# Performance work log

Hardware: AMD Instinct MI355X
Metric: run time of the kernel (lower is better)

Reference implementation:

```python
import jax, jax.numpy as jnp
import numpy as np

N_NODES = 50000


def _gcn_conv(x, W, b, src, dst, norm, n_nodes):
    # x: [N, Fin], W: [Fin, Fout]
    h = x @ W                                   # [N, Fout]
    msg = h[src] * norm[:, None]                # [E+N, Fout] edge messages
    out = jax.ops.segment_sum(msg, dst, num_segments=n_nodes)
    return out + b


def reference(x, edge_index, W1, b1, W2, b2):
    n = x.shape[0]
    # add self-loops (PyG GCNConv default add_self_loops=True)
    loop = jnp.arange(n, dtype=edge_index.dtype)
    src = jnp.concatenate([edge_index[0], loop])
    dst = jnp.concatenate([edge_index[1], loop])
    # symmetric degree normalization: deg over destination with unit weights
    deg = jax.ops.segment_sum(jnp.ones_like(dst, dtype=x.dtype), dst, num_segments=n)
    dinv = jnp.where(deg > 0, jax.lax.rsqrt(deg), 0.0)
    norm = dinv[src] * dinv[dst]                # [E+N]
    h = _gcn_conv(x, W1, b1, src, dst, norm, n)
    h = jax.nn.relu(h)
    out = _gcn_conv(h, W2, b2, src, dst, norm, n)
    return out


def setup_inputs() -> dict:
    key = jax.random.key(0)
    k1, k2, k3, k4 = jax.random.split(key, 4)
    n, e, fin, hid, fout = N_NODES, 800000, 128, 128, 64
    x = jax.random.normal(k1, (n, fin), dtype=jnp.float32)
    edge_index = jax.random.randint(k2, (2, e), 0, n, dtype=jnp.int64)
    # Glorot-ish init for linear weights, zero bias (PyG default)
    W1 = jax.random.normal(k3, (fin, hid), dtype=jnp.float32) / np.sqrt(fin)
    b1 = jnp.zeros((hid,), dtype=jnp.float32)
    W2 = jax.random.normal(k4, (hid, fout), dtype=jnp.float32) / np.sqrt(hid)
    b2 = jnp.zeros((fout,), dtype=jnp.float32)
    return {"x": x, "edge_index": edge_index, "W1": W1, "b1": b1, "W2": W2, "b2": b2}
```

## Files before the change

### kernel.cpp

```cpp
#include <hip/hip_runtime.h>
#include <hip/hip_bf16.h>


constexpr int FIN = 128;
constexpr int HID = 128;
constexpr int FOUT = 64;
constexpr int CAP = 48;
constexpr int NPB = 128;
constexpr int BCAP = 3072;
constexpr int OVF_MAX = 65536;

typedef __attribute__((ext_vector_type(8))) short s16x8;
typedef __attribute__((ext_vector_type(4))) float f32x4;
typedef __attribute__((ext_vector_type(2))) float f32x2;

static __device__ __forceinline__ float bf2f(__hip_bfloat16 v) { return __bfloat162float(v); }
static __device__ __forceinline__ float lo2f(unsigned u) { union { unsigned i; float f; } c; c.i = u << 16; return c.f; }
static __device__ __forceinline__ float hi2f(unsigned u) { union { unsigned i; float f; } c; c.i = u & 0xffff0000u; return c.f; }
static __device__ __forceinline__ unsigned short f2bfu(float f) {
    __hip_bfloat16 h = __float2bfloat16(f);
    union { __hip_bfloat16 h; unsigned short u; } c; c.h = h; return c.u;
}
static __device__ __forceinline__ unsigned pack2(float a, float b) {
    return (unsigned)f2bfu(a) | ((unsigned)f2bfu(b) << 16);
}
static __device__ __forceinline__ f32x2 unpk(unsigned u) {
    union { unsigned i; float f; } a, b;
    a.i = u << 16; b.i = u & 0xffff0000u;
    f32x2 r; r[0] = a.f; r[1] = b.f; return r;
}
static __device__ __forceinline__ void acc_add(f32x2* acc, uint4 v) {
    acc[0] += unpk(v.x); acc[1] += unpk(v.y);
    acc[2] += unpk(v.z); acc[3] += unpk(v.w);
}
static __device__ __forceinline__ void acc_fma(f32x2* acc, uint4 v, float w) {
    f32x2 ws; ws[0] = w; ws[1] = w;
    acc[0] += ws * unpk(v.x); acc[1] += ws * unpk(v.y);
    acc[2] += ws * unpk(v.z); acc[3] += ws * unpk(v.w);
}

struct SW { int s; float w; };

__global__ __launch_bounds__(256) void k_detect(const unsigned* __restrict__ xw,
                                                const int* __restrict__ eiw,
                                                int E, int* __restrict__ flags,
                                                int* __restrict__ gcur,
                                                int* __restrict__ cnt, int N, int zero_cnt) {
    if (zero_cnt)
        for (long i = (long)blockIdx.x * 256 + threadIdx.x; i < N; i += (long)gridDim.x * 256)
            cnt[i] = 0;
    if (blockIdx.x != 0) return;
    for (int i = threadIdx.x; i < 514; i += 256) gcur[i] = 0;
    __shared__ int s_bf16like, s_oddnz;
    if (threadIdx.x == 0) { s_bf16like = 0; s_oddnz = 0; }
    __syncthreads();
    int c = 0;
    for (int i = threadIdx.x; i < 4096; i += 256) {
        unsigned ex = ((xw[i] & 0xffffu) >> 7) & 0xffu;
        if (ex >= 117u && ex <= 130u) c++;
    }
    atomicAdd(&s_bf16like, c);
    int nz = 0;
    for (int i = threadIdx.x; i < 2048; i += 256)
        if (eiw[2 * i + 1] != 0) nz++;
    atomicAdd(&s_oddnz, nz);
    __syncthreads();
    if (threadIdx.x == 0) {
        flags[0] = (s_bf16like < 2048) ? 1 : 0;
        flags[1] = (s_oddnz == 0) ? 1 : 0;
    }
}

__global__ __launch_bounds__(256) void k_mega(const void* __restrict__ Xp,
                                              const void* __restrict__ Wp,
                                              const int* __restrict__ ei, int E, int N,
                                              int nbuk, int GB,
                                              int* __restrict__ gcur,
                                              unsigned* __restrict__ pairs,
                                              int2* __restrict__ ovfA,
                                              int* __restrict__ ovfAcnt,
                                              __hip_bfloat16* __restrict__ G,
                                              const int* __restrict__ flags) {
    extern __shared__ __align__(16) char smem[];
    const int tid = threadIdx.x;
    if ((int)blockIdx.x < GB) {
        short* Wt = (short*)smem;
        const bool f32m = flags[0] != 0;
        for (int i = tid; i < 128 * 128; i += 256) {
            int k = i >> 7, n = i & 127;
            float wv = f32m ? ((const float*)Wp)[(long)k * 128 + n]
                            : bf2f(((const __hip_bfloat16*)Wp)[(long)k * 128 + n]);
            Wt[n * 136 + k] = (short)f2bfu(wv);
        }
        __syncthreads();
        const int w = tid >> 6, lane = tid & 63;
        const int m = lane & 15, quad = lane >> 4;
        const int rowA = blockIdx.x * 64 + w * 16 + m;
        const int rowc = rowA < N ? rowA : N - 1;
        s16x8 afr[4];
#pragma unroll
        for (int kc = 0; kc < 4; ++kc) {
            const int k0 = kc * 32 + quad * 8;
            if (!f32m) {
                afr[kc] = *(const s16x8*)((const __hip_bfloat16*)Xp + (long)rowc * 128 + k0);
            } else {
                const float* p = (const float*)Xp + (long)rowc * 128 + k0;
                s16x8 t;
#pragma unroll
                for (int j = 0; j < 8; ++j) t[j] = (short)f2bfu(p[j]);
                afr[kc] = t;
            }
        }
        const int rbase = blockIdx.x * 64 + w * 16 + quad * 4;
#pragma unroll
        for (int ct = 0; ct < 8; ++ct) {
            f32x4 acc = {0.f, 0.f, 0.f, 0.f};
#pragma unroll
            for (int kc = 0; kc < 4; ++kc) {
                s16x8 bfr = *(const s16x8*)&Wt[(ct * 16 + m) * 136 + kc * 32 + quad * 8];
                acc = __builtin_amdgcn_mfma_f32_16x16x32_bf16(afr[kc], bfr, acc, 0, 0, 0);
            }
            const int plane = ct >> 2;
            const int cp = (ct & 3) * 16 + m;
#pragma unroll
            for (int r = 0; r < 4; ++r) {
                int rr = rbase + r;
                if (rr < N)
                    G[(long)plane * N * 64 + (long)rr * 64 + cp] = __float2bfloat16(acc[r]);
            }
        }
    } else {
        int* hist  = (int*)smem;
        int* gbase = hist + 512;
        int* lofs  = gbase + 512;
        int* cur   = lofs + 513;
        unsigned* buf = (unsigned*)(cur + 512);
        const long base = (long)(blockIdx.x - GB) * 2048;
        const bool i64 = flags[1] != 0;
        int se[8], de[8];
        for (int b = tid; b < nbuk; b += 256) hist[b] = 0;
        __syncthreads();
#pragma unroll
        for (int j = 0; j < 8; ++j) {
            long i = base + j * 256 + tid;
            int s = 0, d = -1;
            if (i < E) {
                if (i64) { s = ((const int2*)ei)[i].x; d = ((const int2*)(ei + 2 * (long)E))[i].x; }
                else     { s = ei[i]; d = ei[(long)E + i]; }
                if ((unsigned)s >= (unsigned)N || (unsigned)d >= (unsigned)N) d = -1;
            }
            se[j] = s; de[j] = d;
            if (d >= 0) atomicAdd(&hist[d / NPB], 1);
        }
        __syncthreads();
        if (tid == 0) {
            int r = 0;
            for (int b = 0; b < nbuk; ++b) { lofs[b] = r; r += hist[b]; }
            lofs[nbuk] = r;
        }
        __syncthreads();
        for (int b = tid; b < nbuk; b += 256) {
            cur[b] = lofs[b];
            int h = hist[b];
            gbase[b] = h > 0 ? atomicAdd(&gcur[b], h) : 0;
        }
        __syncthreads();
#pragma unroll
        for (int j = 0; j < 8; ++j) {
            int d = de[j];
            if (d < 0) continue;
            int b = d / NPB;
            int lp = atomicAdd(&cur[b], 1);
            buf[lp] = ((unsigned)(d - b * NPB) << 16) | (unsigned)se[j];
        }
        __syncthreads();
        const int total = lofs[nbuk];
        for (int i = tid; i < total; i += 256) {
            int lo = 0, hi = nbuk;
            while (hi - lo > 1) { int mid = (lo + hi) >> 1; if (lofs[mid] <= i) lo = mid; else hi = mid; }
            const int b = lo;
            const unsigned val = buf[i];
            const int gp = gbase[b] + (i - lofs[b]);
            if (gp < BCAP) {
                pairs[(long)b * BCAP + gp] = val;
            } else {
                int op = atomicAdd(ovfAcnt, 1);
                if (op < OVF_MAX)
                    ovfA[op] = make_int2(b * NPB + (int)(val >> 16), (int)(val & 0xffffu));
            }
        }
    }
}

__global__ __launch_bounds__(256) void k_binB(const int* __restrict__ gcur,
                                              const unsigned* __restrict__ pairs,
                                              const int2* __restrict__ ovfA,
                                              const int* __restrict__ ovfAcnt,
                                              int* __restrict__ cnt,
                                              float* __restrict__ dinv,
                                              unsigned short* __restrict__ slots,
                                              int2* __restrict__ ovf2,
                                              int* __restrict__ ovf2cnt, int N) {
    __shared__ int cntL[NPB];
    __shared__ __align__(16) unsigned short slotsL[NPB * CAP];
    const int b = blockIdx.x;
    const int tid = threadIdx.x;
    const int d0 = b * NPB;
    const int nd = min(NPB, N - d0);
    if (nd <= 0) return;
    for (int i = tid; i < NPB; i += 256) cntL[i] = 0;
    __syncthreads();
    const int c = min(gcur[b], BCAP);
    const unsigned* pb = pairs + (long)b * BCAP;
    for (int i = tid; i < c; i += 256) {
        unsigned p = pb[i];
        int ld = p >> 16;
        int pos = atomicAdd(&cntL[ld], 1);
        if (pos < CAP) {
            slotsL[ld * CAP + pos] = (unsigned short)(p & 0xffffu);
        } else {
            int op = atomicAdd(ovf2cnt, 1);
            if (op < OVF_MAX) ovf2[op] = make_int2(d0 + ld, (int)(p & 0xffffu));
        }
    }
    int na = *ovfAcnt; na = na < OVF_MAX ? na : OVF_MAX;
    for (int i = tid; i < na; i += 256) {
        int2 p = ovfA[i];
        int ld = p.x - d0;
        if ((unsigned)ld < (unsigned)nd) {
            int pos = atomicAdd(&cntL[ld], 1);
            if (pos < CAP) {
                slotsL[ld * CAP + pos] = (unsigned short)p.y;
            } else {
                int op = atomicAdd(ovf2cnt, 1);
                if (op < OVF_MAX) ovf2[op] = p;
            }
        }
    }
    __syncthreads();
    for (int i = tid; i < nd; i += 256) {
        cnt[d0 + i] = cntL[i];
        dinv[d0 + i] = rsqrtf((float)(cntL[i] + 1));
    }
    const uint4* sv = (const uint4*)slotsL;
    uint4* gv = (uint4*)(slots + (long)d0 * CAP);
    const int total8 = (nd * CAP) >> 3;
    for (int i = tid; i < total8; i += 256) gv[i] = sv[i];
}

__global__ __launch_bounds__(256) void k_build_direct(const int* __restrict__ ei, int E, int N,
                                                      int* __restrict__ cnt,
                                                      int* __restrict__ slots,
                                                      int2* __restrict__ ovf2,
                                                      int* __restrict__ ovf2cnt,
                                                      const int* __restrict__ flags) {
    long i = (long)blockIdx.x * 256 + threadIdx.x;
    if (i >= E) return;
    int s, d;
    if (flags[1]) { s = ((const int2*)ei)[i].x; d = ((const int2*)(ei + 2 * (long)E))[i].x; }
    else          { s = ei[i]; d = ei[(long)E + i]; }
    if ((unsigned)s >= (unsigned)N || (unsigned)d >= (unsigned)N) return;
    int pos = atomicAdd(&cnt[d], 1);
    if (pos < CAP) {
        slots[(long)d * CAP + pos] = s;
    } else {
        int op = atomicAdd(ovf2cnt, 1);
        if (op < OVF_MAX) ovf2[op] = make_int2(d, s);
    }
}

template<int CT, int SPLIT>
__global__ __launch_bounds__(256) void k_gemm(const void* __restrict__ Xp, int x_follows_flag,
                                              const void* __restrict__ Wp,
                                              const int* __restrict__ cnt,
                                              __hip_bfloat16* __restrict__ G,
                                              const int* __restrict__ flags, int N) {
    constexpr int C = CT * 16;
    __shared__ __align__(16) short Wt[C * 136];
    const bool f32m = flags[0] != 0;
    const bool xf32 = (x_follows_flag != 0) && f32m;
    const int tid = threadIdx.x;
    for (int i = tid; i < 128 * C; i += 256) {
        int k = i / C, n = i % C;
        float wv = f32m ? ((const float*)Wp)[(long)k * C + n]
                        : bf2f(((const __hip_bfloat16*)Wp)[(long)k * C + n]);
        Wt[n * 136 + k] = (short)f2bfu(wv);
    }
    __syncthreads();
    const int w = tid >> 6, lane = tid & 63;
    const int m = lane & 15, quad = lane >> 4;
    const int rowA = blockIdx.x * 64 + w * 16 + m;
    const int rowc = rowA < N ? rowA : N - 1;
    s16x8 afr[4];
#pragma unroll
    for (int kc = 0; kc < 4; ++kc) {
        const int k0 = kc * 32 + quad * 8;
        if (!xf32) {
            afr[kc] = *(const s16x8*)((const __hip_bfloat16*)Xp + (long)rowc * 128 + k0);
        } else {
            const float* p = (const float*)Xp + (long)rowc * 128 + k0;
            s16x8 t;
#pragma unroll
            for (int j = 0; j < 8; ++j) t[j] = (short)f2bfu(p[j]);
            afr[kc] = t;
        }
    }
    const int rbase = blockIdx.x * 64 + w * 16 + quad * 4;
    float dv[4];
#pragma unroll
    for (int r = 0; r < 4; ++r) {
        int rr = min(rbase + r, N - 1);
        dv[r] = rsqrtf((float)(cnt[rr] + 1));
    }
#pragma unroll
    for (int ct = 0; ct < CT; ++ct) {
        f32x4 acc = {0.f, 0.f, 0.f, 0.f};
#pragma unroll
        for (int kc = 0; kc < 4; ++kc) {
            s16x8 bfr = *(const s16x8*)&Wt[(ct * 16 + m) * 136 + kc * 32 + quad * 8];
            acc = __builtin_amdgcn_mfma_f32_16x16x32_bf16(afr[kc], bfr, acc, 0, 0, 0);
        }
#pragma unroll
        for (int r = 0; r < 4; ++r) {
            int rr = rbase + r;
            if (rr < N) {
                long off;
                if (SPLIT) {
                    const int plane = ct / (CT / 2);
                    const int cp = (ct % (CT / 2)) * 16 + m;
                    off = (long)plane * N * (C / 2) + (long)rr * (C / 2) + cp;
                } else {
                    off = (long)rr * C + ct * 16 + m;
                }
                G[off] = __float2bfloat16(dv[r] * acc[r]);
            }
        }
    }
}

__global__ __launch_bounds__(256) void k_gather1b(const __hip_bfloat16* __restrict__ G,
                                                  const int* __restrict__ cnt,
                                                  const float* __restrict__ dinv,
                                                  const unsigned short* __restrict__ slots,
                                                  const int2* __restrict__ ovf2,
                                                  const int* __restrict__ ovf2cnt,
                                                  const void* __restrict__ b1,
                                                  __hip_bfloat16* __restrict__ h1,
                                                  const int* __restrict__ flags, int N) {
    __shared__ int cntL[32];
    __shared__ float wsL[32];
    __shared__ __align__(16) SW swL[32 * 49];
    const int tid = threadIdx.x;
    const int n0 = blockIdx.x * 32;
    const int nd = min(32, N - n0);
    for (int i = tid; i < nd; i += 256) {
        cntL[i] = cnt[n0 + i];
        wsL[i] = dinv[n0 + i];
    }
    __syncthreads();
    for (int j = tid; j < 32 * CAP; j += 256) {
        const int ni = j / CAP, sl = j - ni * CAP;
        if (ni < nd) {
            const int mm = min(cntL[ni], CAP);
            if (sl < mm) {
                const int s = slots[(long)(n0 + ni) * CAP + sl];
                swL[ni * 49 + sl].s = s;
                swL[ni * 49 + sl].w = dinv[s];
            }
        }
    }
    __syncthreads();
    const int grp = tid >> 3, lane = tid & 7;
    if (grp >= nd) return;
    const int node = n0 + grp;
    const int cd = cntL[grp];
    const int m = cd < CAP ? cd : CAP;
    const float wself = wsL[grp];
    const SW* sw = &swL[grp * 49];
    const bool f32m = flags[0] != 0;
    for (int P = 0; P < 2; ++P) {
        const __hip_bfloat16* Gp = G + (long)P * N * 64;
        f32x2 acc2[4] = {};
        float* acc = (float*)acc2;
        acc_fma(acc2, ((const uint4*)(Gp + (long)node * 64))[lane], wself);
        int i = 0;
        for (; i + 7 < m; i += 8) {
            SW a0 = sw[i], a1 = sw[i + 1], a2 = sw[i + 2], a3 = sw[i + 3];
            SW a4 = sw[i + 4], a5 = sw[i + 5], a6 = sw[i + 6], a7 = sw[i + 7];
            uint4 v0 = ((const uint4*)(Gp + (long)a0.s * 64))[lane];
            uint4 v1 = ((const uint4*)(Gp + (long)a1.s * 64))[lane];
            uint4 v2 = ((const uint4*)(Gp + (long)a2.s * 64))[lane];
            uint4 v3 = ((const uint4*)(Gp + (long)a3.s * 64))[lane];
            uint4 v4 = ((const uint4*)(Gp + (long)a4.s * 64))[lane];
            uint4 v5 = ((const uint4*)(Gp + (long)a5.s * 64))[lane];
            uint4 v6 = ((const uint4*)(Gp + (long)a6.s * 64))[lane];
            uint4 v7 = ((const uint4*)(Gp + (long)a7.s * 64))[lane];
            acc_fma(acc2, v0, a0.w); acc_fma(acc2, v1, a1.w);
            acc_fma(acc2, v2, a2.w); acc_fma(acc2, v3, a3.w);
            acc_fma(acc2, v4, a4.w); acc_fma(acc2, v5, a5.w);
            acc_fma(acc2, v6, a6.w); acc_fma(acc2, v7, a7.w);
        }
        for (; i + 3 < m; i += 4) {
            SW a0 = sw[i], a1 = sw[i + 1], a2 = sw[i + 2], a3 = sw[i + 3];
            uint4 v0 = ((const uint4*)(Gp + (long)a0.s * 64))[lane];
            uint4 v1 = ((const uint4*)(Gp + (long)a1.s * 64))[lane];
            uint4 v2 = ((const uint4*)(Gp + (long)a2.s * 64))[lane];
            uint4 v3 = ((const uint4*)(Gp + (long)a3.s * 64))[lane];
            acc_fma(acc2, v0, a0.w); acc_fma(acc2, v1, a1.w);
            acc_fma(acc2, v2, a2.w); acc_fma(acc2, v3, a3.w);
        }
        for (; i < m; ++i) {
            SW a = sw[i];
            acc_fma(acc2, ((const uint4*)(Gp + (long)a.s * 64))[lane], a.w);
        }
        if (cd > CAP) {
            int oc = *ovf2cnt; oc = oc < OVF_MAX ? oc : OVF_MAX;
            for (int j = 0; j < oc; ++j)
                if (ovf2[j].x == node) {
                    int s0 = ovf2[j].y;
                    acc_fma(acc2, ((const uint4*)(Gp + (long)s0 * 64))[lane], dinv[s0]);
                }
        }
        const int c0 = P * 64 + lane * 8;
        float bv[8];
        if (f32m) {
            const float4* bp = (const float4*)((const float*)b1 + c0);
            float4 b0 = bp[0], b1v = bp[1];
            bv[0] = b0.x; bv[1] = b0.y; bv[2] = b0.z; bv[3] = b0.w;
            bv[4] = b1v.x; bv[5] = b1v.y; bv[6] = b1v.z; bv[7] = b1v.w;
        } else {
            uint4 b = *(const uint4*)((const __hip_bfloat16*)b1 + c0);
            bv[0] = lo2f(b.x); bv[1] = hi2f(b.x); bv[2] = lo2f(b.y); bv[3] = hi2f(b.y);
            bv[4] = lo2f(b.z); bv[5] = hi2f(b.z); bv[6] = lo2f(b.w); bv[7] = hi2f(b.w);
        }
        float o[8];
#pragma unroll
        for (int c = 0; c < 8; ++c) {
            float v = wself * acc[c] + bv[c];
            o[c] = v > 0.f ? v : 0.f;
        }
        uint4 pv = { pack2(o[0], o[1]), pack2(o[2], o[3]), pack2(o[4], o[5]), pack2(o[6], o[7]) };
        ((uint4*)(h1 + (long)node * 128 + P * 64))[lane] = pv;
    }
}

template<int F, int LAYER1, typename ST>
__global__ __launch_bounds__(256) void k_gather(const __hip_bfloat16* __restrict__ G,
                                                const int* __restrict__ cnt,
                                                const ST* __restrict__ slots,
                                                const int2* __restrict__ ovf2,
                                                const int* __restrict__ ovf2cnt,
                                                const void* __restrict__ bias,
                                                void* __restrict__ outp,
                                                const int* __restrict__ flags, int N) {
    constexpr int L = F / 8;
    constexpr int NODES = 256 / L;
    const int tid = threadIdx.x;
    const int grp = tid / L, lane = tid % L;
    const int node = blockIdx.x * NODES + grp;
    if (node >= N) return;
    const int cd = cnt[node];
    const float wself = rsqrtf((float)(cd + 1));
    const int m = cd < CAP ? cd : CAP;
    const ST* sl = slots + (long)node * CAP;
    f32x2 acc2[4] = {};
    float* acc = (float*)acc2;
    acc_add(acc2, ((const uint4*)(G + (long)node * F))[lane]);
    int i = 0;
    for (; i + 7 < m; i += 8) {
        int s0 = sl[i], s1 = sl[i + 1], s2 = sl[i + 2], s3 = sl[i + 3];
        int s4 = sl[i + 4], s5 = sl[i + 5], s6 = sl[i + 6], s7 = sl[i + 7];
        uint4 v0 = ((const uint4*)(G + (long)s0 * F))[lane];
        uint4 v1 = ((const uint4*)(G + (long)s1 * F))[lane];
        uint4 v2 = ((const uint4*)(G + (long)s2 * F))[lane];
        uint4 v3 = ((const uint4*)(G + (long)s3 * F))[lane];
        uint4 v4 = ((const uint4*)(G + (long)s4 * F))[lane];
        uint4 v5 = ((const uint4*)(G + (long)s5 * F))[lane];
        uint4 v6 = ((const uint4*)(G + (long)s6 * F))[lane];
        uint4 v7 = ((const uint4*)(G + (long)s7 * F))[lane];
        acc_add(acc2, v0); acc_add(acc2, v1); acc_add(acc2, v2); acc_add(acc2, v3);
        acc_add(acc2, v4); acc_add(acc2, v5); acc_add(acc2, v6); acc_add(acc2, v7);
    }
    for (; i + 3 < m; i += 4) {
        int s0 = sl[i], s1 = sl[i + 1], s2 = sl[i + 2], s3 = sl[i + 3];
        uint4 v0 = ((const uint4*)(G + (long)s0 * F))[lane];
        uint4 v1 = ((const uint4*)(G + (long)s1 * F))[lane];
        uint4 v2 = ((const uint4*)(G + (long)s2 * F))[lane];
        uint4 v3 = ((const uint4*)(G + (long)s3 * F))[lane];
        acc_add(acc2, v0); acc_add(acc2, v1); acc_add(acc2, v2); acc_add(acc2, v3);
    }
    for (; i < m; ++i)
        acc_add(acc2, ((const uint4*)(G + (long)sl[i] * F))[lane]);
    if (cd > CAP) {
        int oc = *ovf2cnt; oc = oc < OVF_MAX ? oc : OVF_MAX;
        for (int j = 0; j < oc; ++j)
            if (ovf2[j].x == node)
                acc_add(acc2, ((const uint4*)(G + (long)ovf2[j].y * F))[lane]);
    }
    const bool f32m = flags[0] != 0;
    const int c0 = lane * 8;
    float bv[8];
    if (f32m) {
        const float4* bp = (const float4*)((const float*)bias + c0);
        float4 b0 = bp[0], b1 = bp[1];
        bv[0] = b0.x; bv[1] = b0.y; bv[2] = b0.z; bv[3] = b0.w;
        bv[4] = b1.x; bv[5] = b1.y; bv[6] = b1.z; bv[7] = b1.w;
    } else {
        uint4 b = *(const uint4*)((const __hip_bfloat16*)bias + c0);
        bv[0] = lo2f(b.x); bv[1] = hi2f(b.x); bv[2] = lo2f(b.y); bv[3] = hi2f(b.y);
        bv[4] = lo2f(b.z); bv[5] = hi2f(b.z); bv[6] = lo2f(b.w); bv[7] = hi2f(b.w);
    }
    float o[8];
#pragma unroll
    for (int c = 0; c < 8; ++c) {
        float v = wself * acc[c] + bv[c];
        o[c] = (LAYER1 && v < 0.f) ? 0.f : v;
    }
    if (LAYER1 || !f32m) {
        uint4 pv = { pack2(o[0], o[1]), pack2(o[2], o[3]), pack2(o[4], o[5]), pack2(o[6], o[7]) };
        ((uint4*)outp)[(long)node * L + lane] = pv;
    } else {
        float4* op = (float4*)((float*)outp + (long)node * F + c0);
        op[0] = make_float4(o[0], o[1], o[2], o[3]);
        op[1] = make_float4(o[4], o[5], o[6], o[7]);
    }
}

extern "C" void kernel_launch(void* const* d_in, const int* in_sizes, int n_in,
                              void* d_out, int out_size, void* d_ws, size_t ws_size,
                              hipStream_t stream) {
    const void* x  = d_in[0];
    const int*  ei = (const int*)d_in[1];
    const void* W1 = d_in[2];
    const void* b1 = d_in[3];
    const void* W2 = d_in[4];
    const void* b2 = d_in[5];

    const int N = in_sizes[0] / FIN;
    const int E = in_sizes[1] / 2;
    const int nbuk = (N + NPB - 1) / NPB;

    char* ws = (char*)d_ws;
    int*   flags   = (int*)ws;
    int*   gcur    = (int*)(ws + 4096);
    int*   ovfAcnt = gcur + 512;
    int*   ovf2cnt = gcur + 513;
    int*   cnt     = (int*)(ws + 65536);
    float* dinv    = (float*)(ws + 266240);
    int2*  ovfA    = (int2*)(ws + 524288);
    int2*  ovf2    = (int2*)(ws + 1048576);
    unsigned short* slots16 = (unsigned short*)(ws + 2097152);
    int*   slots32 = (int*)(ws + 2097152);
    __hip_bfloat16* g  = (__hip_bfloat16*)(ws + 11730944);
    __hip_bfloat16* g2 = g;
    unsigned* pairs = (unsigned*)(ws + 24530944);
    __hip_bfloat16* h1 = (__hip_bfloat16*)(ws + 24530944);

    const int GB = (N + 63) / 64;
    const int AB = (E + 2047) / 2048;
    const int EB = (E + 255) / 256;

    if (N <= 65536 && nbuk <= 512) {
        k_detect<<<1, 256, 0, stream>>>((const unsigned*)x, ei, E, flags, gcur, cnt, N, 0);
        k_mega<<<GB + AB, 256, 34816, stream>>>(x, W1, ei, E, N, nbuk, GB,
                                                gcur, pairs, ovfA, ovfAcnt, g, flags);
        k_binB<<<nbuk, 256, 0, stream>>>(gcur, pairs, ovfA, ovfAcnt, cnt, dinv, slots16, ovf2, ovf2cnt, N);
        const int GBL = (N + 31) / 32;
        k_gather1b<<<GBL, 256, 0, stream>>>(g, cnt, dinv, slots16, ovf2, ovf2cnt, b1, h1, flags, N);
        k_gemm<4, 0><<<GB, 256, 0, stream>>>(h1, 0, W2, cnt, g2, flags, N);
        k_gather<64, 0, unsigned short><<<(N + 31) / 32, 256, 0, stream>>>(
            g2, cnt, slots16, ovf2, ovf2cnt, b2, d_out, flags, N);
    } else {
        k_detect<<<64, 256, 0, stream>>>((const unsigned*)x, ei, E, flags, gcur, cnt, N, 1);
        k_build_direct<<<EB, 256, 0, stream>>>(ei, E, N, cnt, slots32, ovf2, ovf2cnt, flags);
        k_gemm<8, 0><<<GB, 256, 0, stream>>>(x, 1, W1, cnt, g, flags, N);
        k_gather<128, 1, int><<<(N + 15) / 16, 256, 0, stream>>>(
            g, cnt, slots32, ovf2, ovf2cnt, b1, h1, flags, N);
        k_gemm<4, 0><<<GB, 256, 0, stream>>>(h1, 0, W2, cnt, g2, flags, N);
        k_gather<64, 0, int><<<(N + 31) / 32, 256, 0, stream>>>(
            g2, cnt, slots16 ? (const int*)slots32 : (const int*)slots32, ovf2, ovf2cnt, b2, d_out, flags, N);
    }
}
```

Baseline: 202.9 us.

## Replace two-pass bucketed CSR build with direct global-atomic slot insertion

```diff
diff --git a/kernel.cpp b/kernel.cpp
--- a/kernel.cpp
+++ b/kernel.cpp
@@ -6,8 +6,6 @@
 constexpr int HID = 128;
 constexpr int FOUT = 64;
 constexpr int CAP = 48;
-constexpr int NPB = 128;
-constexpr int BCAP = 3072;
 constexpr int OVF_MAX = 65536;
 
 typedef __attribute__((ext_vector_type(8))) short s16x8;
@@ -45,10 +43,9 @@
                                                 const int* __restrict__ eiw,
                                                 int E, int* __restrict__ flags,
                                                 int* __restrict__ gcur,
-                                                int* __restrict__ cnt, int N, int zero_cnt) {
-    if (zero_cnt)
-        for (long i = (long)blockIdx.x * 256 + threadIdx.x; i < N; i += (long)gridDim.x * 256)
-            cnt[i] = 0;
+                                                int* __restrict__ cnt, int N) {
+    for (long i = (long)blockIdx.x * 256 + threadIdx.x; i < N; i += (long)gridDim.x * 256)
+        cnt[i] = 0;
     if (blockIdx.x != 0) return;
     for (int i = threadIdx.x; i < 514; i += 256) gcur[i] = 0;
     __shared__ int s_bf16like, s_oddnz;
@@ -74,11 +71,11 @@
 __global__ __launch_bounds__(256) void k_mega(const void* __restrict__ Xp,
                                               const void* __restrict__ Wp,
                                               const int* __restrict__ ei, int E, int N,
-                                              int nbuk, int GB,
-                                              int* __restrict__ gcur,
-                                              unsigned* __restrict__ pairs,
-                                              int2* __restrict__ ovfA,
-                                              int* __restrict__ ovfAcnt,
+                                              int GB,
+                                              int* __restrict__ cnt,
+                                              unsigned short* __restrict__ slots,
+                                              int2* __restrict__ ovf2,
+                                              int* __restrict__ ovf2cnt,
                                               __hip_bfloat16* __restrict__ G,
                                               const int* __restrict__ flags) {
     extern __shared__ __align__(16) char smem[];
@@ -130,16 +127,9 @@
             }
         }
     } else {
-        int* hist  = (int*)smem;
-        int* gbase = hist + 512;
-        int* lofs  = gbase + 512;
-        int* cur   = lofs + 513;
-        unsigned* buf = (unsigned*)(cur + 512);
         const long base = (long)(blockIdx.x - GB) * 2048;
         const bool i64 = flags[1] != 0;
         int se[8], de[8];
-        for (int b = tid; b < nbuk; b += 256) hist[b] = 0;
-        __syncthreads();
 #pragma unroll
         for (int j = 0; j < 8; ++j) {
             long i = base + j * 256 + tid;
@@ -150,102 +140,26 @@
                 if ((unsigned)s >= (unsigned)N || (unsigned)d >= (unsigned)N) d = -1;
             }
             se[j] = s; de[j] = d;
-            if (d >= 0) atomicAdd(&hist[d / NPB], 1);
-        }
-        __syncthreads();
-        if (tid == 0) {
-            int r = 0;
-            for (int b = 0; b < nbuk; ++b) { lofs[b] = r; r += hist[b]; }
-            lofs[nbuk] = r;
-        }
-        __syncthreads();
-        for (int b = tid; b < nbuk; b += 256) {
-            cur[b] = lofs[b];
-            int h = hist[b];
-            gbase[b] = h > 0 ? atomicAdd(&gcur[b], h) : 0;
-        }
-        __syncthreads();
+        }
 #pragma unroll
         for (int j = 0; j < 8; ++j) {
-            int d = de[j];
+            const int d = de[j];
             if (d < 0) continue;
-            int b = d / NPB;
-            int lp = atomicAdd(&cur[b], 1);
-            buf[lp] = ((unsigned)(d - b * NPB) << 16) | (unsigned)se[j];
-        }
-        __syncthreads();
-        const int total = lofs[nbuk];
-        for (int i = tid; i < total; i += 256) {
-            int lo = 0, hi = nbuk;
-            while (hi - lo > 1) { int mid = (lo + hi) >> 1; if (lofs[mid] <= i) lo = mid; else hi = mid; }
-            const int b = lo;
-            const unsigned val = buf[i];
-            const int gp = gbase[b] + (i - lofs[b]);
-            if (gp < BCAP) {
-                pairs[(long)b * BCAP + gp] = val;
-            } else {
-                int op = atomicAdd(ovfAcnt, 1);
-                if (op < OVF_MAX)
-                    ovfA[op] = make_int2(b * NPB + (int)(val >> 16), (int)(val & 0xffffu));
-            }
-        }
-    }
-}
-
-__global__ __launch_bounds__(256) void k_binB(const int* __restrict__ gcur,
-                                              const unsigned* __restrict__ pairs,
-                                              const int2* __restrict__ ovfA,
-                                              const int* __restrict__ ovfAcnt,
-                                              int* __restrict__ cnt,
-                                              float* __restrict__ dinv,
-                                              unsigned short* __restrict__ slots,
-                                              int2* __restrict__ ovf2,
-                                              int* __restrict__ ovf2cnt, int N) {
-    __shared__ int cntL[NPB];
-    __shared__ __align__(16) unsigned short slotsL[NPB * CAP];
-    const int b = blockIdx.x;
-    const int tid = threadIdx.x;
-    const int d0 = b * NPB;
-    const int nd = min(NPB, N - d0);
-    if (nd <= 0) return;
-    for (int i = tid; i < NPB; i += 256) cntL[i] = 0;
-    __syncthreads();
-    const int c = min(gcur[b], BCAP);
-    const unsigned* pb = pairs + (long)b * BCAP;
-    for (int i = tid; i < c; i += 256) {
-        unsigned p = pb[i];
-        int ld = p >> 16;
-        int pos = atomicAdd(&cntL[ld], 1);
-        if (pos < CAP) {
-            slotsL[ld * CAP + pos] = (unsigned short)(p & 0xffffu);
-        } else {
-            int op = atomicAdd(ovf2cnt, 1);
-            if (op < OVF_MAX) ovf2[op] = make_int2(d0 + ld, (int)(p & 0xffffu));
-        }
-    }
-    int na = *ovfAcnt; na = na < OVF_MAX ? na : OVF_MAX;
-    for (int i = tid; i < na; i += 256) {
-        int2 p = ovfA[i];
-        int ld = p.x - d0;
-        if ((unsigned)ld < (unsigned)nd) {
-            int pos = atomicAdd(&cntL[ld], 1);
+            const int pos = atomicAdd(&cnt[d], 1);
             if (pos < CAP) {
-                slotsL[ld * CAP + pos] = (unsigned short)p.y;
+                slots[(long)d * CAP + pos] = (unsigned short)se[j];
             } else {
                 int op = atomicAdd(ovf2cnt, 1);
-                if (op < OVF_MAX) ovf2[op] = p;
-            }
-        }
-    }
-    __syncthreads();
-    for (int i = tid; i < nd; i += 256) {
-        cnt[d0 + i] = cntL[i];
-        dinv[d0 + i] = rsqrtf((float)(cntL[i] + 1));
-    }
-    const uint4* sv = (const uint4*)slotsL;
-    uint4* gv = (uint4*)(slots + (long)d0 * CAP);
-    const int total8 = (nd * CAP) >> 3;
-    for (int i = tid; i < total8; i += 256) gv[i] = sv[i];
+                if (op < OVF_MAX) ovf2[op] = make_int2(d, se[j]);
+            }
+        }
+    }
+}
+
+__global__ __launch_bounds__(256) void k_dinv(const int* __restrict__ cnt,
+                                              float* __restrict__ dinv, int N) {
+    int i = blockIdx.x * 256 + threadIdx.x;
+    if (i < N) dinv[i] = rsqrtf((float)(cnt[i] + 1));
 }
 
 __global__ __launch_bounds__(256) void k_build_direct(const int* __restrict__ ei, int E, int N,
@@ -538,46 +452,42 @@
 
     const int N = in_sizes[0] / FIN;
     const int E = in_sizes[1] / 2;
-    const int nbuk = (N + NPB - 1) / NPB;
 
     char* ws = (char*)d_ws;
     int*   flags   = (int*)ws;
     int*   gcur    = (int*)(ws + 4096);
-    int*   ovfAcnt = gcur + 512;
     int*   ovf2cnt = gcur + 513;
     int*   cnt     = (int*)(ws + 65536);
     float* dinv    = (float*)(ws + 266240);
-    int2*  ovfA    = (int2*)(ws + 524288);
     int2*  ovf2    = (int2*)(ws + 1048576);
     unsigned short* slots16 = (unsigned short*)(ws + 2097152);
     int*   slots32 = (int*)(ws + 2097152);
     __hip_bfloat16* g  = (__hip_bfloat16*)(ws + 11730944);
     __hip_bfloat16* g2 = g;
-    unsigned* pairs = (unsigned*)(ws + 24530944);
     __hip_bfloat16* h1 = (__hip_bfloat16*)(ws + 24530944);
 
     const int GB = (N + 63) / 64;
     const int AB = (E + 2047) / 2048;
     const int EB = (E + 255) / 256;
 
-    if (N <= 65536 && nbuk <= 512) {
-        k_detect<<<1, 256, 0, stream>>>((const unsigned*)x, ei, E, flags, gcur, cnt, N, 0);
-        k_mega<<<GB + AB, 256, 34816, stream>>>(x, W1, ei, E, N, nbuk, GB,
-                                                gcur, pairs, ovfA, ovfAcnt, g, flags);
-        k_binB<<<nbuk, 256, 0, stream>>>(gcur, pairs, ovfA, ovfAcnt, cnt, dinv, slots16, ovf2, ovf2cnt, N);
+    if (N <= 65536) {
+        k_detect<<<64, 256, 0, stream>>>((const unsigned*)x, ei, E, flags, gcur, cnt, N);
+        k_mega<<<GB + AB, 256, 34816, stream>>>(x, W1, ei, E, N, GB,
+                                                cnt, slots16, ovf2, ovf2cnt, g, flags);
+        k_dinv<<<(N + 255) / 256, 256, 0, stream>>>(cnt, dinv, N);
         const int GBL = (N + 31) / 32;
         k_gather1b<<<GBL, 256, 0, stream>>>(g, cnt, dinv, slots16, ovf2, ovf2cnt, b1, h1, flags, N);
         k_gemm<4, 0><<<GB, 256, 0, stream>>>(h1, 0, W2, cnt, g2, flags, N);
         k_gather<64, 0, unsigned short><<<(N + 31) / 32, 256, 0, stream>>>(
             g2, cnt, slots16, ovf2, ovf2cnt, b2, d_out, flags, N);
     } else {
-        k_detect<<<64, 256, 0, stream>>>((const unsigned*)x, ei, E, flags, gcur, cnt, N, 1);
+        k_detect<<<64, 256, 0, stream>>>((const unsigned*)x, ei, E, flags, gcur, cnt, N);
         k_build_direct<<<EB, 256, 0, stream>>>(ei, E, N, cnt, slots32, ovf2, ovf2cnt, flags);
         k_gemm<8, 0><<<GB, 256, 0, stream>>>(x, 1, W1, cnt, g, flags, N);
         k_gather<128, 1, int><<<(N + 15) / 16, 256, 0, stream>>>(
             g, cnt, slots32, ovf2, ovf2cnt, b1, h1, flags, N);
         k_gemm<4, 0><<<GB, 256, 0, stream>>>(h1, 0, W2, cnt, g2, flags, N);
         k_gather<64, 0, int><<<(N + 31) / 32, 256, 0, stream>>>(
-            g2, cnt, slots16 ? (const int*)slots32 : (const int*)slots32, ovf2, ovf2cnt, b2, d_out, flags, N);
-    }
-}
+            g2, cnt, slots32, ovf2, ovf2cnt, b2, d_out, flags, N);
+    }
+}
```

New measurement: 211.6 us. 4.3% more time.

## Scatter edges directly to global bins, sort per-node slot lists, shrink bucket size

Applied to the files above, without the earlier changes.

```diff
diff --git a/kernel.cpp b/kernel.cpp
--- a/kernel.cpp
+++ b/kernel.cpp
@@ -6,7 +6,7 @@
 constexpr int HID = 128;
 constexpr int FOUT = 64;
 constexpr int CAP = 48;
-constexpr int NPB = 128;
+constexpr int NPB = 98;
 constexpr int BCAP = 3072;
 constexpr int OVF_MAX = 65536;
 
@@ -130,11 +130,8 @@
             }
         }
     } else {
-        int* hist  = (int*)smem;
+        int* hist = (int*)smem;
         int* gbase = hist + 512;
-        int* lofs  = gbase + 512;
-        int* cur   = lofs + 513;
-        unsigned* buf = (unsigned*)(cur + 512);
         const long base = (long)(blockIdx.x - GB) * 2048;
         const bool i64 = flags[1] != 0;
         int se[8], de[8];
@@ -153,16 +150,10 @@
             if (d >= 0) atomicAdd(&hist[d / NPB], 1);
         }
         __syncthreads();
-        if (tid == 0) {
-            int r = 0;
-            for (int b = 0; b < nbuk; ++b) { lofs[b] = r; r += hist[b]; }
-            lofs[nbuk] = r;
-        }
-        __syncthreads();
         for (int b = tid; b < nbuk; b += 256) {
-            cur[b] = lofs[b];
             int h = hist[b];
             gbase[b] = h > 0 ? atomicAdd(&gcur[b], h) : 0;
+            hist[b] = 0;
         }
         __syncthreads();
 #pragma unroll
@@ -170,23 +161,12 @@
             int d = de[j];
             if (d < 0) continue;
             int b = d / NPB;
-            int lp = atomicAdd(&cur[b], 1);
-            buf[lp] = ((unsigned)(d - b * NPB) << 16) | (unsigned)se[j];
-        }
-        __syncthreads();
-        const int total = lofs[nbuk];
-        for (int i = tid; i < total; i += 256) {
-            int lo = 0, hi = nbuk;
-            while (hi - lo > 1) { int mid = (lo + hi) >> 1; if (lofs[mid] <= i) lo = mid; else hi = mid; }
-            const int b = lo;
-            const unsigned val = buf[i];
-            const int gp = gbase[b] + (i - lofs[b]);
-            if (gp < BCAP) {
-                pairs[(long)b * BCAP + gp] = val;
+            int p = gbase[b] + atomicAdd(&hist[b], 1);
+            if (p < BCAP) {
+                pairs[(long)b * BCAP + p] = ((unsigned)(d - b * NPB) << 16) | (unsigned)se[j];
             } else {
                 int op = atomicAdd(ovfAcnt, 1);
-                if (op < OVF_MAX)
-                    ovfA[op] = make_int2(b * NPB + (int)(val >> 16), (int)(val & 0xffffu));
+                if (op < OVF_MAX) ovfA[op] = make_int2(d, se[j]);
             }
         }
     }
@@ -235,6 +215,17 @@
                 int op = atomicAdd(ovf2cnt, 1);
                 if (op < OVF_MAX) ovf2[op] = p;
             }
+        }
+    }
+    __syncthreads();
+    for (int ld = tid; ld < nd; ld += 256) {
+        const int mloc = min(cntL[ld], CAP);
+        unsigned short* row = &slotsL[ld * CAP];
+        for (int a = 1; a < mloc; ++a) {
+            const unsigned short key = row[a];
+            int p = a - 1;
+            while (p >= 0 && row[p] > key) { row[p + 1] = row[p]; --p; }
+            row[p + 1] = key;
         }
     }
     __syncthreads();
@@ -578,6 +569,6 @@
             g, cnt, slots32, ovf2, ovf2cnt, b1, h1, flags, N);
         k_gemm<4, 0><<<GB, 256, 0, stream>>>(h1, 0, W2, cnt, g2, flags, N);
         k_gather<64, 0, int><<<(N + 31) / 32, 256, 0, stream>>>(
-            g2, cnt, slots16 ? (const int*)slots32 : (const int*)slots32, ovf2, ovf2cnt, b2, d_out, flags, N);
-    }
-}
+            g2, cnt, slots32, ovf2, ovf2cnt, b2, d_out, flags, N);
+    }
+}
```

Result: slower. 232.6 us (+14.7%).
